# Kernel tuning notes

Measured on AMD Instinct MI355X. Metric: run time of the kernel, lower is better.

Reference implementation:

```python
import jax, jax.numpy as jnp
import numpy as np

EPS = 1e-05  # matches torch module default eps
B, F = 32768, 1024


def setup_inputs() -> dict:
    key = jax.random.key(0)
    x = jax.random.normal(key, (B, F), dtype=jnp.float32)
    M = jnp.zeros((F,), jnp.float32)  # running mean buffer (_M), _n = 0 at init
    S = jnp.zeros((F,), jnp.float32)  # running M2 buffer (_S)
    return {"x": x, "M": M, "S": S}


def _welford(M, S, x):
    """Sequential Welford update over the batch dim, exactly mirroring push()."""
    def step(carry, xi):
        M, S, n = carry
        n1 = n
        n = n + 1
        nf = n.astype(xi.dtype)
        delta = xi - M
        first = n == 1  # first sample ever: M <- x, S unchanged
        M_new = jnp.where(first, xi, M + delta / nf)
        S_new = jnp.where(first, S, S + delta * delta * (n1.astype(xi.dtype) / nf))
        return (M_new, S_new, n), None

    (M, S, n), _ = jax.lax.scan(step, (M, S, jnp.int32(0)), x)
    return M, S, n


def reference(x, M, S):
    M, S, n = _welford(M, S, x)
    nf = n.astype(x.dtype)
    # var = S / (n - 1) if n > 1 else M**2  (module's .var property)
    var = jnp.where(n > 1, S / (nf - 1.0), jnp.square(M))
    # running stats are requires_grad=False buffers in torch -> constants
    mean = jax.lax.stop_gradient(M)
    std = jax.lax.stop_gradient(jnp.sqrt(var))
    return (x - mean) / (std + EPS)
```

## Files before the change

### kernel.cpp

```cpp
#include <hip/hip_runtime.h>
#include <math.h>

#define NFEAT 1024
#define NROWS 32768
#define EPS 1e-5f

#define NB1 1024
#define RPB1 (NROWS / NB1)
#define FG (NFEAT / 4)
#define NB3 2048
#define RPB3 (NROWS / NB3)

typedef float f32x4 __attribute__((ext_vector_type(4)));


__global__ __launch_bounds__(256) void reduce_kernel(
    const float* __restrict__ x,
    float* __restrict__ sums, float* __restrict__ sumsq)
{
    const int t = threadIdx.x;
    const size_t base = (size_t)(blockIdx.x * RPB1) * FG + t;
    const f32x4* xv = (const f32x4*)x;

    f32x4 s = {0.f, 0.f, 0.f, 0.f};
    f32x4 q = {0.f, 0.f, 0.f, 0.f};

    #pragma unroll
    for (int r = 0; r < RPB1; r += 4) {
        f32x4 v0 = xv[base + (size_t)(r + 0) * FG];
        f32x4 v1 = xv[base + (size_t)(r + 1) * FG];
        f32x4 v2 = xv[base + (size_t)(r + 2) * FG];
        f32x4 v3 = xv[base + (size_t)(r + 3) * FG];
        s += v0 + v1 + v2 + v3;
        q += v0 * v0 + v1 * v1 + v2 * v2 + v3 * v3;
    }

    const int c = 4 * t;
    atomicAdd(&sums[c + 0], s.x);  atomicAdd(&sums[c + 1], s.y);
    atomicAdd(&sums[c + 2], s.z);  atomicAdd(&sums[c + 3], s.w);
    atomicAdd(&sumsq[c + 0], q.x); atomicAdd(&sumsq[c + 1], q.y);
    atomicAdd(&sumsq[c + 2], q.z); atomicAdd(&sumsq[c + 3], q.w);
}

__global__ __launch_bounds__(256) void norm_kernel(
    const float* __restrict__ x,
    const float* __restrict__ sums, const float* __restrict__ sumsq,
    float* __restrict__ out)
{
    const int t = threadIdx.x;
    const size_t base = (size_t)(blockIdx.x * RPB3) * FG + t;
    const f32x4* xv = (const f32x4*)x;
    f32x4* ov = (f32x4*)out;

    f32x4 S = ((const f32x4*)sums)[t];
    f32x4 Q = ((const f32x4*)sumsq)[t];
    const float n   = (float)NROWS;
    const float rn  = 1.0f / n;
    const float rn1 = 1.0f / (n - 1.0f);
    f32x4 m, iv;
    m = S * rn;
    iv.x = 1.0f / (sqrtf((Q.x - S.x * S.x * rn) * rn1) + EPS);
    iv.y = 1.0f / (sqrtf((Q.y - S.y * S.y * rn) * rn1) + EPS);
    iv.z = 1.0f / (sqrtf((Q.z - S.z * S.z * rn) * rn1) + EPS);
    iv.w = 1.0f / (sqrtf((Q.w - S.w * S.w * rn) * rn1) + EPS);

    #pragma unroll
    for (int r = 0; r < RPB3; r += 4) {
        f32x4 v0 = xv[base + (size_t)(r + 0) * FG];
        f32x4 v1 = xv[base + (size_t)(r + 1) * FG];
        f32x4 v2 = xv[base + (size_t)(r + 2) * FG];
        f32x4 v3 = xv[base + (size_t)(r + 3) * FG];
        f32x4 o0 = (v0 - m) * iv;
        f32x4 o1 = (v1 - m) * iv;
        f32x4 o2 = (v2 - m) * iv;
        f32x4 o3 = (v3 - m) * iv;
        __builtin_nontemporal_store(o0, &ov[base + (size_t)(r + 0) * FG]);
        __builtin_nontemporal_store(o1, &ov[base + (size_t)(r + 1) * FG]);
        __builtin_nontemporal_store(o2, &ov[base + (size_t)(r + 2) * FG]);
        __builtin_nontemporal_store(o3, &ov[base + (size_t)(r + 3) * FG]);
    }
}

extern "C" void kernel_launch(void* const* d_in, const int* in_sizes, int n_in,
                              void* d_out, int out_size, void* d_ws, size_t ws_size,
                              hipStream_t stream) {
    const float* x = (const float*)d_in[0];
    float* out = (float*)d_out;

    float* sums  = (float*)d_ws;
    float* sumsq = sums + NFEAT;

    hipMemsetAsync(d_ws, 0, 2 * NFEAT * sizeof(float), stream);
    reduce_kernel<<<NB1, 256, 0, stream>>>(x, sums, sumsq);
    norm_kernel<<<NB3, 256, 0, stream>>>(x, sums, sumsq, out);
}
```

Measured before the change: 326.9 us.

## Replace atomic column reduction with two-pass partial-sum reduction

Removes the float atomicAdds and the workspace memset. The first kernel now writes per-block partial sums and sums of squares into workspace, and a second kernel tree-reduces them per column group and precomputes mean and inverse std once. The normalize kernel then just loads those two vectors. It also doubles the first-pass block count, unrolls by 8, and adds an occupancy hint. In exchange it writes and reads about 16 MB of partials and adds one more kernel launch.

```diff
diff --git a/kernel.cpp b/kernel.cpp
--- a/kernel.cpp
+++ b/kernel.cpp
@@ -5,18 +5,18 @@
 #define NROWS 32768
 #define EPS 1e-5f
 
-#define NB1 1024
+#define NB1 2048
 #define RPB1 (NROWS / NB1)
 #define FG (NFEAT / 4)
+#define NB2 FG
 #define NB3 2048
 #define RPB3 (NROWS / NB3)
 
 typedef float f32x4 __attribute__((ext_vector_type(4)));
 
 
-__global__ __launch_bounds__(256) void reduce_kernel(
-    const float* __restrict__ x,
-    float* __restrict__ sums, float* __restrict__ sumsq)
+__global__ __launch_bounds__(256, 8) void reduce1_kernel(
+    const float* __restrict__ x, f32x4* __restrict__ ps, f32x4* __restrict__ pq)
 {
     const int t = threadIdx.x;
     const size_t base = (size_t)(blockIdx.x * RPB1) * FG + t;
@@ -26,25 +26,69 @@
     f32x4 q = {0.f, 0.f, 0.f, 0.f};
 
     #pragma unroll
-    for (int r = 0; r < RPB1; r += 4) {
-        f32x4 v0 = xv[base + (size_t)(r + 0) * FG];
-        f32x4 v1 = xv[base + (size_t)(r + 1) * FG];
-        f32x4 v2 = xv[base + (size_t)(r + 2) * FG];
-        f32x4 v3 = xv[base + (size_t)(r + 3) * FG];
-        s += v0 + v1 + v2 + v3;
-        q += v0 * v0 + v1 * v1 + v2 * v2 + v3 * v3;
+    for (int rr = 0; rr < RPB1; rr += 8) {
+        f32x4 v0 = xv[base + (size_t)(rr + 0) * FG];
+        f32x4 v1 = xv[base + (size_t)(rr + 1) * FG];
+        f32x4 v2 = xv[base + (size_t)(rr + 2) * FG];
+        f32x4 v3 = xv[base + (size_t)(rr + 3) * FG];
+        f32x4 v4 = xv[base + (size_t)(rr + 4) * FG];
+        f32x4 v5 = xv[base + (size_t)(rr + 5) * FG];
+        f32x4 v6 = xv[base + (size_t)(rr + 6) * FG];
+        f32x4 v7 = xv[base + (size_t)(rr + 7) * FG];
+        s += ((v0 + v1) + (v2 + v3)) + ((v4 + v5) + (v6 + v7));
+        q += ((v0 * v0 + v1 * v1) + (v2 * v2 + v3 * v3))
+           + ((v4 * v4 + v5 * v5) + (v6 * v6 + v7 * v7));
+    }
+    ps[(size_t)blockIdx.x * FG + t] = s;
+    pq[(size_t)blockIdx.x * FG + t] = q;
+}
+
+__global__ __launch_bounds__(256) void reduce2_kernel(
+    const f32x4* __restrict__ ps, const f32x4* __restrict__ pq,
+    f32x4* __restrict__ mean, f32x4* __restrict__ inv)
+{
+    const int t = threadIdx.x;
+    const int cgi = blockIdx.x;
+
+    f32x4 s = {0.f, 0.f, 0.f, 0.f};
+    f32x4 q = {0.f, 0.f, 0.f, 0.f};
+    #pragma unroll
+    for (int k = 0; k < NB1 / 256; ++k) {
+        s += ps[(size_t)(t + 256 * k) * FG + cgi];
+        q += pq[(size_t)(t + 256 * k) * FG + cgi];
     }
 
-    const int c = 4 * t;
-    atomicAdd(&sums[c + 0], s.x);  atomicAdd(&sums[c + 1], s.y);
-    atomicAdd(&sums[c + 2], s.z);  atomicAdd(&sums[c + 3], s.w);
-    atomicAdd(&sumsq[c + 0], q.x); atomicAdd(&sumsq[c + 1], q.y);
-    atomicAdd(&sumsq[c + 2], q.z); atomicAdd(&sumsq[c + 3], q.w);
+    __shared__ f32x4 ls[256];
+    __shared__ f32x4 lq[256];
+    ls[t] = s; lq[t] = q;
+    __syncthreads();
+    #pragma unroll
+    for (int off = 128; off > 0; off >>= 1) {
+        if (t < off) {
+            ls[t] += ls[t + off];
+            lq[t] += lq[t + off];
+        }
+        __syncthreads();
+    }
+
+    if (t == 0) {
+        f32x4 S = ls[0], Q = lq[0];
+        const float n   = (float)NROWS;
+        const float rn  = 1.0f / n;
+        const float rn1 = 1.0f / (n - 1.0f);
+        f32x4 m = S * rn, iv;
+        iv.x = 1.0f / (sqrtf((Q.x - S.x * S.x * rn) * rn1) + EPS);
+        iv.y = 1.0f / (sqrtf((Q.y - S.y * S.y * rn) * rn1) + EPS);
+        iv.z = 1.0f / (sqrtf((Q.z - S.z * S.z * rn) * rn1) + EPS);
+        iv.w = 1.0f / (sqrtf((Q.w - S.w * S.w * rn) * rn1) + EPS);
+        mean[cgi] = m;
+        inv[cgi]  = iv;
+    }
 }
 
 __global__ __launch_bounds__(256) void norm_kernel(
     const float* __restrict__ x,
-    const float* __restrict__ sums, const float* __restrict__ sumsq,
+    const f32x4* __restrict__ mean, const f32x4* __restrict__ inv,
     float* __restrict__ out)
 {
     const int t = threadIdx.x;
@@ -52,17 +96,8 @@
     const f32x4* xv = (const f32x4*)x;
     f32x4* ov = (f32x4*)out;
 
-    f32x4 S = ((const f32x4*)sums)[t];
-    f32x4 Q = ((const f32x4*)sumsq)[t];
-    const float n   = (float)NROWS;
-    const float rn  = 1.0f / n;
-    const float rn1 = 1.0f / (n - 1.0f);
-    f32x4 m, iv;
-    m = S * rn;
-    iv.x = 1.0f / (sqrtf((Q.x - S.x * S.x * rn) * rn1) + EPS);
-    iv.y = 1.0f / (sqrtf((Q.y - S.y * S.y * rn) * rn1) + EPS);
-    iv.z = 1.0f / (sqrtf((Q.z - S.z * S.z * rn) * rn1) + EPS);
-    iv.w = 1.0f / (sqrtf((Q.w - S.w * S.w * rn) * rn1) + EPS);
+    const f32x4 m  = mean[t];
+    const f32x4 iv = inv[t];
 
     #pragma unroll
     for (int r = 0; r < RPB3; r += 4) {
@@ -87,10 +122,12 @@
     const float* x = (const float*)d_in[0];
     float* out = (float*)d_out;
 
-    float* sums  = (float*)d_ws;
-    float* sumsq = sums + NFEAT;
+    f32x4* mean = (f32x4*)d_ws;
+    f32x4* inv  = mean + FG;
+    f32x4* ps   = inv + FG;
+    f32x4* pq   = ps + (size_t)NB1 * FG;
 
-    hipMemsetAsync(d_ws, 0, 2 * NFEAT * sizeof(float), stream);
-    reduce_kernel<<<NB1, 256, 0, stream>>>(x, sums, sumsq);
-    norm_kernel<<<NB3, 256, 0, stream>>>(x, sums, sumsq, out);
+    reduce1_kernel<<<NB1, 256, 0, stream>>>(x, ps, pq);
+    reduce2_kernel<<<NB2, 256, 0, stream>>>(ps, pq, mean, inv);
+    norm_kernel<<<NB3, 256, 0, stream>>>(x, mean, inv, out);
 }
```

Result: faster. 276.6 us (-15.4%).
